# Kernel tuning notes

Hardware: AMD Instinct MI355X
Metric: run time of the kernel (lower is better)

Reference implementation:

```python
import jax, jax.numpy as jnp
import numpy as np

LAMBDA_TEMP = 20.0
GAMMA = 20.0
MARGIN = 0.05
EPS = 1e-8

B, K, M, D = 128, 256, 8, 128


def _unit(x, axis=-1):
    return x / jnp.linalg.norm(x, axis=axis, keepdims=True)


def setup_inputs() -> dict:
    key = jax.random.key(0)
    k1, k2, k3 = jax.random.split(key, 3)
    v_proj = _unit(jax.random.normal(k1, (B, K, D), dtype=jnp.float32))
    prototypes = _unit(jax.random.normal(k2, (K, M, D), dtype=jnp.float32))
    concept_labels = jax.random.randint(k3, (B, K), 0, 2, dtype=jnp.int64)
    return {"v_proj": v_proj, "concept_labels": concept_labels, "prototypes": prototypes}


def reference(v_proj, concept_labels, prototypes):
    # all-pairs prototype similarities: query vector (b,k) vs prototypes of concept c
    # sims: (B, K, C, M)
    sims = jnp.einsum('bkd,cmd->bkcm', v_proj, prototypes)
    # Eq.6: soft assignment over the M prototypes of each concept
    q = jax.nn.softmax(GAMMA * sims, axis=-1)
    # Eq.7-8: weighted similarity sim_c(v)  -> (B, K, C)
    sim = jnp.sum(q * sims, axis=-1)
    # positive similarity: concept k queried against its own prototypes, plus margin
    sim_pos = jnp.einsum('bkk->bk', sim) + MARGIN  # (B, K)
    # Eq.9: -log( exp(lam*sim_pos) / (sum_c exp(lam*sim_c) + eps) )
    denom = jnp.sum(jnp.exp(LAMBDA_TEMP * sim), axis=-1) + EPS  # (B, K)
    loss_bk = jnp.log(denom) - LAMBDA_TEMP * sim_pos  # (B, K)
    mask = (concept_labels == 1).astype(loss_bk.dtype)
    num_pos = jnp.sum(mask)
    total = jnp.sum(loss_bk * mask)
    return jnp.where(num_pos > 0, total / num_pos, total)
```

## Files before the change

kernel.cpp:

```cpp
#include <hip/hip_runtime.h>

#define LT      20.0f
#define LN2     0.69314718055994531f
#define C2EXP   28.853900817779268f
#define CHUNKS  16
#define NBLK    512
#define PW_COPY 262144

typedef _Float16 half8 __attribute__((ext_vector_type(8)));
typedef float    f32x4 __attribute__((ext_vector_type(4)));

#if __has_builtin(__builtin_amdgcn_exp2f)
#define EXP2F(x) __builtin_amdgcn_exp2f(x)
#else
#define EXP2F(x) __expf(0.69314718055994531f * (x))
#endif

__device__ __forceinline__ float swz16(float x) {
    return __int_as_float(__builtin_amdgcn_ds_swizzle(__float_as_int(x), 0x401F));
}

#define GLD16(gp, lp) __builtin_amdgcn_global_load_lds( \
    (const __attribute__((address_space(1))) void*)(gp), \
    (__attribute__((address_space(3))) void*)(lp), 16, 0, 0)

__global__ __launch_bounds__(256)
void mpcl_prep(const float* __restrict__ P, _Float16* __restrict__ Pw,
               int* __restrict__ ws)
{
    if (blockIdx.x == 0 && threadIdx.x == 0) ws[0] = 0;
    int copy = blockIdx.x & 7;
    int id   = (blockIdx.x >> 3) * 256 + threadIdx.x;
    int ch    = id >> 11;
    int colq  = (id >> 9) & 3;
    int cfrag = (id >> 6) & 7;
    int lane  = id & 63;
    int n = lane & 15, q = lane >> 4;
    int c = cfrag & 3, h = cfrag >> 2;
    int col  = colq * 32 + ((n >> 2) << 3) + (n & 3) + (h << 2);
    int gcol = (ch << 7) + col;
    const float* src = P + ((size_t)gcol << 7) + c * 32 + q * 8;
    float4 a = *(const float4*)src;
    float4 b = *(const float4*)(src + 4);
    half8 hv;
    hv[0] = (_Float16)(C2EXP * a.x); hv[1] = (_Float16)(C2EXP * a.y);
    hv[2] = (_Float16)(C2EXP * a.z); hv[3] = (_Float16)(C2EXP * a.w);
    hv[4] = (_Float16)(C2EXP * b.x); hv[5] = (_Float16)(C2EXP * b.y);
    hv[6] = (_Float16)(C2EXP * b.z); hv[7] = (_Float16)(C2EXP * b.w);
    *(half8*)(Pw + (size_t)copy * PW_COPY + (size_t)id * 8) = hv;
}

__global__ __attribute__((amdgpu_flat_work_group_size(512, 512),
                          amdgpu_waves_per_eu(4, 4)))
void mpcl_main(const float* __restrict__ V,
               const int*   __restrict__ labels,
               const _Float16* __restrict__ Pw,
               int* __restrict__ ws,
               float* __restrict__ out)
{
    __shared__ __align__(16) _Float16 Pst[2][2048 * 8];
    __shared__ float sh_denom[64];
    __shared__ float sh_simpos[64];
    __shared__ float sh_fin[16];
    __shared__ int   sh_last;

    int*   gcnt = ws;
    float* part = (float*)((char*)ws + 256);

    const int tid  = threadIdx.x;
    const int lane = tid & 63;
    const int w    = tid >> 6;
    const int colq = w & 3;
    const int rg   = w >> 2;
    const int n    = lane & 15;
    const int q    = lane >> 4;
    const int rowbase = blockIdx.x * 64;

    if (tid < 64) { sh_denom[tid] = 0.0f; sh_simpos[tid] = 0.0f; }

    int lab = 0;
    if (tid < 64) lab = labels[rowbase + tid];

    const _Float16* gbase = Pw + (size_t)(blockIdx.x & 7) * PW_COPY
                               + (size_t)(w * 256 + lane) * 8;

#define STAGE(CH, B) do {                                       \
    const _Float16* g_ = gbase + (size_t)(CH) * 16384;          \
    _Float16* l_ = &Pst[B][(w * 256) * 8];                      \
    GLD16(g_,        l_);                                       \
    GLD16(g_ +  512, l_ +  512);                                \
    GLD16(g_ + 1024, l_ + 1024);                                \
    GLD16(g_ + 1536, l_ + 1536);                                \
} while (0)

    half8 vh[2][4];
#pragma unroll
    for (int rf = 0; rf < 2; ++rf) {
        const float* vr = V + ((size_t)(rowbase + rg * 32 + rf * 16 + n) << 7) + q * 8;
#pragma unroll
        for (int c = 0; c < 4; ++c) {
            float4 x0 = *(const float4*)(vr + c * 32);
            float4 x1 = *(const float4*)(vr + c * 32 + 4);
            vh[rf][c][0] = (_Float16)x0.x; vh[rf][c][1] = (_Float16)x0.y;
            vh[rf][c][2] = (_Float16)x0.z; vh[rf][c][3] = (_Float16)x0.w;
            vh[rf][c][4] = (_Float16)x1.x; vh[rf][c][5] = (_Float16)x1.y;
            vh[rf][c][6] = (_Float16)x1.z; vh[rf][c][7] = (_Float16)x1.w;
        }
    }

    __syncthreads();

    STAGE(0, 0);
    STAGE(1, 1);

    const int rowk0 = (rowbase + rg * 32 + n) & 255;
    const int rowk1 = (rowbase + rg * 32 + 16 + n) & 255;
    const int aoff  = (colq * 512 + lane) * 8;

    float dn0 = 0.f, dn1 = 0.f;
    int cA = colq * 4 + q;

#pragma unroll 1
    for (int ch = 0; ch < CHUNKS; ++ch) {
        if (ch < CHUNKS - 1) asm volatile("s_waitcnt vmcnt(4)" ::: "memory");
        else                 asm volatile("s_waitcnt vmcnt(0)" ::: "memory");
        __builtin_amdgcn_s_barrier();

        const _Float16* base = &Pst[ch & 1][0];

        f32x4 acc1[2] = {{0.f,0.f,0.f,0.f},{0.f,0.f,0.f,0.f}};
        f32x4 acc2[2] = {{0.f,0.f,0.f,0.f},{0.f,0.f,0.f,0.f}};
#pragma unroll
        for (int c = 0; c < 4; ++c) {
            half8 a1 = *(const half8*)&base[aoff + c * 512];
            half8 a2 = *(const half8*)&base[aoff + c * 512 + 2048];
            acc1[0] = __builtin_amdgcn_mfma_f32_16x16x32_f16(a1, vh[0][c], acc1[0], 0, 0, 0);
            acc1[1] = __builtin_amdgcn_mfma_f32_16x16x32_f16(a1, vh[1][c], acc1[1], 0, 0, 0);
            acc2[0] = __builtin_amdgcn_mfma_f32_16x16x32_f16(a2, vh[0][c], acc2[0], 0, 0, 0);
            acc2[1] = __builtin_amdgcn_mfma_f32_16x16x32_f16(a2, vh[1][c], acc2[1], 0, 0, 0);
        }

#pragma unroll
        for (int rf = 0; rf < 2; ++rf) {
            float x0 = acc1[rf][0], x1 = acc1[rf][1], x2 = acc1[rf][2], x3 = acc1[rf][3];
            float x4 = acc2[rf][0], x5 = acc2[rf][1], x6 = acc2[rf][2], x7 = acc2[rf][3];
            float e0 = EXP2F(x0), e1 = EXP2F(x1), e2 = EXP2F(x2), e3 = EXP2F(x3);
            float e4 = EXP2F(x4), e5 = EXP2F(x5), e6 = EXP2F(x6), e7 = EXP2F(x7);
            float es = ((e0 + e1) + (e2 + e3)) + ((e4 + e5) + (e6 + e7));
            float ss = fmaf(e0, x0, fmaf(e1, x1, fmaf(e2, x2, e3 * x3)))
                     + fmaf(e4, x4, fmaf(e5, x5, fmaf(e6, x6, e7 * x7)));
            float simY = __fdividef(ss, es);
            if (rf) dn1 += EXP2F(simY); else dn0 += EXP2F(simY);
            if (cA == (rf ? rowk1 : rowk0))
                sh_simpos[rg * 32 + rf * 16 + n] = simY;
        }
        cA += 16;

        __builtin_amdgcn_s_barrier();
        if (ch + 2 < CHUNKS) STAGE(ch + 2, ch & 1);
    }

#pragma unroll
    for (int rf = 0; rf < 2; ++rf) {
        float t = rf ? dn1 : dn0;
        t += swz16(t);
        t += __shfl_xor(t, 32);
        if (lane < 16)
            atomicAdd(&sh_denom[rg * 32 + rf * 16 + n], t);
    }
    __syncthreads();

    float s = 0.f, cc = 0.f;
    if (tid < 64) {
        float lp = logf(sh_denom[tid] + 1e-8f) - LN2 * sh_simpos[tid] - 1.0f;
        float mk = (lab == 1) ? 1.0f : 0.0f;
        s = lp * mk;
        cc = mk;
    }
#pragma unroll
    for (int off = 32; off >= 1; off >>= 1) {
        s  += __shfl_down(s, off);
        cc += __shfl_down(cc, off);
    }

    if (tid == 0) {
        __hip_atomic_store(&part[2 * blockIdx.x],     s,  __ATOMIC_RELAXED, __HIP_MEMORY_SCOPE_AGENT);
        __hip_atomic_store(&part[2 * blockIdx.x + 1], cc, __ATOMIC_RELAXED, __HIP_MEMORY_SCOPE_AGENT);
        __threadfence();
        int g = __hip_atomic_fetch_add(gcnt, 1, __ATOMIC_ACQ_REL, __HIP_MEMORY_SCOPE_AGENT);
        sh_last = (g == NBLK - 1);
    }
    __syncthreads();
    if (sh_last) {
        float ts = 0.f, tc = 0.f;
        for (int i = tid; i < NBLK; i += 512) {
            ts += __hip_atomic_load(&part[2 * i],     __ATOMIC_RELAXED, __HIP_MEMORY_SCOPE_AGENT);
            tc += __hip_atomic_load(&part[2 * i + 1], __ATOMIC_RELAXED, __HIP_MEMORY_SCOPE_AGENT);
        }
#pragma unroll
        for (int off = 32; off >= 1; off >>= 1) {
            ts += __shfl_down(ts, off);
            tc += __shfl_down(tc, off);
        }
        if (lane == 0) { sh_fin[w] = ts; sh_fin[8 + w] = tc; }
        __syncthreads();
        if (tid == 0) {
            ts = 0.f; tc = 0.f;
#pragma unroll
            for (int i = 0; i < 8; ++i) { ts += sh_fin[i]; tc += sh_fin[8 + i]; }
            out[0] = (tc > 0.0f) ? (ts / tc) : ts;
        }
    }
}

extern "C" void kernel_launch(void* const* d_in, const int* in_sizes, int n_in,
                              void* d_out, int out_size, void* d_ws, size_t ws_size,
                              hipStream_t stream)
{
    const float* V      = (const float*)d_in[0];
    const int*   labels = (const int*)d_in[1];
    const float* P      = (const float*)d_in[2];
    float* out = (float*)d_out;
    int*   ws  = (int*)d_ws;
    _Float16* Pw = (_Float16*)((char*)d_ws + 16384);

    mpcl_prep<<<1024, 256, 0, stream>>>(P, Pw, ws);
    mpcl_main<<<NBLK, 512, 0, stream>>>(V, labels, Pw, ws, out);
}
```

Before: 109.9 us.

## Halve rows per block, double grid, and drop LDS double buffering

Each block now handles 32 query rows instead of 64, and the grid grows to 1024 blocks. Prototype staging goes from a two-buffer prefetch pipeline to a single LDS buffer that is loaded and waited on inside every chunk. The smaller LDS footprint and the new launch bounds are meant to allow more resident blocks, so latency is hidden by occupancy instead of explicit prefetch. The cost is that every block still streams the full prototype set, so total prototype traffic through LDS doubles, each LDS load feeds half as many MFMAs, and each chunk waits on its load with no overlap.

Result: slower. 130.2 us (+18.4%).

```diff
diff --git a/kernel.cpp b/kernel.cpp
--- a/kernel.cpp
+++ b/kernel.cpp
@@ -4,7 +4,7 @@
 #define LN2     0.69314718055994531f
 #define C2EXP   28.853900817779268f
 #define CHUNKS  16
-#define NBLK    512
+#define NBLK    1024
 #define PW_COPY 262144
 
 typedef _Float16 half8 __attribute__((ext_vector_type(8)));
@@ -50,17 +50,16 @@
     *(half8*)(Pw + (size_t)copy * PW_COPY + (size_t)id * 8) = hv;
 }
 
-__global__ __attribute__((amdgpu_flat_work_group_size(512, 512),
-                          amdgpu_waves_per_eu(4, 4)))
+__global__ __launch_bounds__(512, 8)
 void mpcl_main(const float* __restrict__ V,
                const int*   __restrict__ labels,
                const _Float16* __restrict__ Pw,
                int* __restrict__ ws,
                float* __restrict__ out)
 {
-    __shared__ __align__(16) _Float16 Pst[2][2048 * 8];
-    __shared__ float sh_denom[64];
-    __shared__ float sh_simpos[64];
+    __shared__ __align__(16) _Float16 Pst[2048 * 8];
+    __shared__ float sh_denom[32];
+    __shared__ float sh_simpos[32];
     __shared__ float sh_fin[16];
     __shared__ int   sh_last;
 
@@ -71,117 +70,101 @@
     const int lane = tid & 63;
     const int w    = tid >> 6;
     const int colq = w & 3;
-    const int rg   = w >> 2;
+    const int rh   = (w >> 2) & 1;
     const int n    = lane & 15;
     const int q    = lane >> 4;
-    const int rowbase = blockIdx.x * 64;
-
-    if (tid < 64) { sh_denom[tid] = 0.0f; sh_simpos[tid] = 0.0f; }
+    const int rowbase = blockIdx.x * 32;
+
+    if (tid < 32) { sh_denom[tid] = 0.0f; sh_simpos[tid] = 0.0f; }
 
     int lab = 0;
-    if (tid < 64) lab = labels[rowbase + tid];
+    if (tid < 32) lab = labels[rowbase + tid];
 
     const _Float16* gbase = Pw + (size_t)(blockIdx.x & 7) * PW_COPY
                                + (size_t)(w * 256 + lane) * 8;
 
-#define STAGE(CH, B) do {                                       \
+#define STAGE(CH) do {                                          \
     const _Float16* g_ = gbase + (size_t)(CH) * 16384;          \
-    _Float16* l_ = &Pst[B][(w * 256) * 8];                      \
+    _Float16* l_ = &Pst[(w * 256) * 8];                         \
     GLD16(g_,        l_);                                       \
     GLD16(g_ +  512, l_ +  512);                                \
     GLD16(g_ + 1024, l_ + 1024);                                \
     GLD16(g_ + 1536, l_ + 1536);                                \
 } while (0)
 
-    half8 vh[2][4];
-#pragma unroll
-    for (int rf = 0; rf < 2; ++rf) {
-        const float* vr = V + ((size_t)(rowbase + rg * 32 + rf * 16 + n) << 7) + q * 8;
+    half8 vh[4];
+    {
+        const float* vr = V + ((size_t)(rowbase + rh * 16 + n) << 7) + q * 8;
 #pragma unroll
         for (int c = 0; c < 4; ++c) {
             float4 x0 = *(const float4*)(vr + c * 32);
             float4 x1 = *(const float4*)(vr + c * 32 + 4);
-            vh[rf][c][0] = (_Float16)x0.x; vh[rf][c][1] = (_Float16)x0.y;
-            vh[rf][c][2] = (_Float16)x0.z; vh[rf][c][3] = (_Float16)x0.w;
-            vh[rf][c][4] = (_Float16)x1.x; vh[rf][c][5] = (_Float16)x1.y;
-            vh[rf][c][6] = (_Float16)x1.z; vh[rf][c][7] = (_Float16)x1.w;
-        }
-    }
-
-    __syncthreads();
-
-    STAGE(0, 0);
-    STAGE(1, 1);
-
-    const int rowk0 = (rowbase + rg * 32 + n) & 255;
-    const int rowk1 = (rowbase + rg * 32 + 16 + n) & 255;
-    const int aoff  = (colq * 512 + lane) * 8;
-
-    float dn0 = 0.f, dn1 = 0.f;
+            vh[c][0] = (_Float16)x0.x; vh[c][1] = (_Float16)x0.y;
+            vh[c][2] = (_Float16)x0.z; vh[c][3] = (_Float16)x0.w;
+            vh[c][4] = (_Float16)x1.x; vh[c][5] = (_Float16)x1.y;
+            vh[c][6] = (_Float16)x1.z; vh[c][7] = (_Float16)x1.w;
+        }
+    }
+
+    const int rowk = (rowbase + rh * 16 + n) & 255;
+    const int aoff = (colq * 512 + lane) * 8;
+
+    float dn = 0.f;
     int cA = colq * 4 + q;
 
 #pragma unroll 1
     for (int ch = 0; ch < CHUNKS; ++ch) {
-        if (ch < CHUNKS - 1) asm volatile("s_waitcnt vmcnt(4)" ::: "memory");
-        else                 asm volatile("s_waitcnt vmcnt(0)" ::: "memory");
-        __builtin_amdgcn_s_barrier();
-
-        const _Float16* base = &Pst[ch & 1][0];
-
-        f32x4 acc1[2] = {{0.f,0.f,0.f,0.f},{0.f,0.f,0.f,0.f}};
-        f32x4 acc2[2] = {{0.f,0.f,0.f,0.f},{0.f,0.f,0.f,0.f}};
+        __syncthreads();
+        STAGE(ch);
+        asm volatile("s_waitcnt vmcnt(0)" ::: "memory");
+        __syncthreads();
+
+        f32x4 acc1 = {0.f, 0.f, 0.f, 0.f};
+        f32x4 acc2 = {0.f, 0.f, 0.f, 0.f};
 #pragma unroll
         for (int c = 0; c < 4; ++c) {
-            half8 a1 = *(const half8*)&base[aoff + c * 512];
-            half8 a2 = *(const half8*)&base[aoff + c * 512 + 2048];
-            acc1[0] = __builtin_amdgcn_mfma_f32_16x16x32_f16(a1, vh[0][c], acc1[0], 0, 0, 0);
-            acc1[1] = __builtin_amdgcn_mfma_f32_16x16x32_f16(a1, vh[1][c], acc1[1], 0, 0, 0);
-            acc2[0] = __builtin_amdgcn_mfma_f32_16x16x32_f16(a2, vh[0][c], acc2[0], 0, 0, 0);
-            acc2[1] = __builtin_amdgcn_mfma_f32_16x16x32_f16(a2, vh[1][c], acc2[1], 0, 0, 0);
-        }
-
-#pragma unroll
-        for (int rf = 0; rf < 2; ++rf) {
-            float x0 = acc1[rf][0], x1 = acc1[rf][1], x2 = acc1[rf][2], x3 = acc1[rf][3];
-            float x4 = acc2[rf][0], x5 = acc2[rf][1], x6 = acc2[rf][2], x7 = acc2[rf][3];
+            half8 a1 = *(const half8*)&Pst[aoff + c * 512];
+            half8 a2 = *(const half8*)&Pst[aoff + c * 512 + 2048];
+            acc1 = __builtin_amdgcn_mfma_f32_16x16x32_f16(a1, vh[c], acc1, 0, 0, 0);
+            acc2 = __builtin_amdgcn_mfma_f32_16x16x32_f16(a2, vh[c], acc2, 0, 0, 0);
+        }
+
+        {
+            float x0 = acc1[0], x1 = acc1[1], x2 = acc1[2], x3 = acc1[3];
+            float x4 = acc2[0], x5 = acc2[1], x6 = acc2[2], x7 = acc2[3];
             float e0 = EXP2F(x0), e1 = EXP2F(x1), e2 = EXP2F(x2), e3 = EXP2F(x3);
             float e4 = EXP2F(x4), e5 = EXP2F(x5), e6 = EXP2F(x6), e7 = EXP2F(x7);
             float es = ((e0 + e1) + (e2 + e3)) + ((e4 + e5) + (e6 + e7));
             float ss = fmaf(e0, x0, fmaf(e1, x1, fmaf(e2, x2, e3 * x3)))
                      + fmaf(e4, x4, fmaf(e5, x5, fmaf(e6, x6, e7 * x7)));
             float simY = __fdividef(ss, es);
-            if (rf) dn1 += EXP2F(simY); else dn0 += EXP2F(simY);
-            if (cA == (rf ? rowk1 : rowk0))
-                sh_simpos[rg * 32 + rf * 16 + n] = simY;
+            dn += EXP2F(simY);
+            if (cA == rowk)
+                sh_simpos[rh * 16 + n] = simY;
         }
         cA += 16;
-
-        __builtin_amdgcn_s_barrier();
-        if (ch + 2 < CHUNKS) STAGE(ch + 2, ch & 1);
-    }
-
-#pragma unroll
-    for (int rf = 0; rf < 2; ++rf) {
-        float t = rf ? dn1 : dn0;
+    }
+
+    {
+        float t = dn;
         t += swz16(t);
         t += __shfl_xor(t, 32);
         if (lane < 16)
-            atomicAdd(&sh_denom[rg * 32 + rf * 16 + n], t);
+            atomicAdd(&sh_denom[rh * 16 + n], t);
     }
     __syncthreads();
 
     float s = 0.f, cc = 0.f;
-    if (tid < 64) {
+    if (tid < 32) {
         float lp = logf(sh_denom[tid] + 1e-8f) - LN2 * sh_simpos[tid] - 1.0f;
         float mk = (lab == 1) ? 1.0f : 0.0f;
         s = lp * mk;
         cc = mk;
     }
 #pragma unroll
-    for (int off = 32; off >= 1; off >>= 1) {
-        s  += __shfl_down(s, off);
-        cc += __shfl_down(cc, off);
-    }
+    for (int off = 16; off >= 1; off >>= 1) s  += __shfl_down(s, off);
+#pragma unroll
+    for (int off = 16; off >= 1; off >>= 1) cc += __shfl_down(cc, off);
 
     if (tid == 0) {
         __hip_atomic_store(&part[2 * blockIdx.x],     s,  __ATOMIC_RELAXED, __HIP_MEMORY_SCOPE_AGENT);
```
